# Performance work log

Measured on AMD Instinct MI355X. Metric: run time of the kernel, lower is better.

## Reference

```python
import jax, jax.numpy as jnp
import numpy as np

H = W = 192
C = 256
MAX_FEATURES = 2048
NUM_UP = 4  # num_upsampling scaling steps: pos -> pos*2 + 0.5 each step

# HandcraftedLocalizationModule filters (D2-Net)
DI  = [[0., -0.5, 0.], [0., 0., 0.], [0., 0.5, 0.]]
DJ  = [[0., 0., 0.], [-0.5, 0., 0.5], [0., 0., 0.]]
DII = [[0., 1., 0.], [0., -2., 0.], [0., 1., 0.]]
DJJ = [[0., 0., 0.], [1., -2., 1.], [0., 0., 0.]]
DIJ = [[0.25, 0., -0.25], [0., 0., 0.], [-0.25, 0., 0.25]]


def _conv3(x, k):
    # x: [H,W]; 3x3 cross-correlation, padding 1 (matches F.conv2d)
    k = jnp.asarray(k, x.dtype)
    return jax.lax.conv_general_dilated(x[None, None], k[None, None],
                                        window_strides=(1, 1),
                                        padding=[(1, 1), (1, 1)])[0, 0]


def _process_scale(feat, score):
    # feat: [C,H,W] dense descriptors, score: [H,W] attention/detection map
    Hm, Wm = score.shape
    # --- NMS: 3x3 maxpool, keep only local maxima (x[lmax != x] = 0) ---
    lmax = jax.lax.reduce_window(score, -jnp.inf, jax.lax.max,
                                 (3, 3), (1, 1), [(1, 1), (1, 1)])
    det = jnp.where(lmax == score, score, 0.0)
    valid = det != 0.0  # torch.nonzero equivalent (fixed-shape mask)
    # --- handcrafted localization (2x2 Newton step on the raw score map) ---
    di, dj = _conv3(score, DI), _conv3(score, DJ)
    dii, djj, dij = _conv3(score, DII), _conv3(score, DJJ), _conv3(score, DIJ)
    dd = dii * djj - dij * dij
    dd = jnp.where(dd == 0.0, 1e-20, dd)  # degenerate Hessian -> huge step, rejected by |.|<0.5
    step_i = -(djj * di - dij * dj) / dd
    step_j = -(-dij * di + dii * dj) / dd
    valid &= (jnp.abs(step_i) < 0.5) & (jnp.abs(step_j) < 0.5)
    ii, jj = jnp.meshgrid(jnp.arange(Hm, dtype=score.dtype),
                          jnp.arange(Wm, dtype=score.dtype), indexing='ij')
    ki = jnp.where(valid, ii + step_i, 0.0)
    kj = jnp.where(valid, jj + step_j, 0.0)
    # --- bilinear interpolation of dense features at sub-pixel keypoints ---
    i0 = jnp.floor(ki)
    j0 = jnp.floor(kj)
    valid &= (i0 >= 0) & (j0 >= 0) & (i0 + 1 <= Hm - 1) & (j0 + 1 <= Wm - 1)
    i0c = jnp.clip(i0, 0, Hm - 2).astype(jnp.int32)
    j0c = jnp.clip(j0, 0, Wm - 2).astype(jnp.int32)
    wi = ki - i0c
    wj = kj - j0c
    desc = (feat[:, i0c, j0c] * (1 - wi) * (1 - wj)
            + feat[:, i0c, j0c + 1] * (1 - wi) * wj
            + feat[:, i0c + 1, j0c] * wi * (1 - wj)
            + feat[:, i0c + 1, j0c + 1] * wi * wj)  # [C,H,W]
    norm = jnp.maximum(jnp.sqrt(jnp.sum(desc * desc, axis=0)), 1e-12)
    desc = desc / norm  # F.normalize(dim=0)
    # --- upscale positions: pos = pos*2 + 0.5 repeated NUM_UP times ---
    for _ in range(NUM_UP):
        ki = ki * 2 + 0.5
        kj = kj * 2 + 0.5
    scores = jnp.where(valid, det, -jnp.inf)  # invalid padded with -inf
    kp = jnp.stack([kj, ki], axis=-1).reshape(-1, 2)  # [:, [1,0]] swap -> (x, y)
    return kp, desc.reshape(desc.shape[0], -1).T, scores.reshape(-1), det


def setup_inputs() -> dict:
    key = jax.random.key(0)
    ks = jax.random.split(key, 6)
    return {
        "feat_early": jax.random.normal(ks[0], (1, C, H, W), jnp.float32),
        "feat_middle": jax.random.normal(ks[1], (1, C, H, W), jnp.float32),
        "feat_deep": jax.random.normal(ks[2], (1, C, H, W), jnp.float32),
        "score_early": jax.random.uniform(ks[3], (1, 1, H, W), jnp.float32),
        "score_middle": jax.random.uniform(ks[4], (1, 1, H, W), jnp.float32),
        "score_deep": jax.random.uniform(ks[5], (1, 1, H, W), jnp.float32),
    }


def reference(feat_early, feat_middle, feat_deep, score_early, score_middle, score_deep):
    feats = [feat_early[0], feat_middle[0], feat_deep[0]]
    smaps = [score_early[0, 0], score_middle[0, 0], score_deep[0, 0]]
    kps, descs, scs, dets = zip(*[_process_scale(f, s) for f, s in zip(feats, smaps)])
    kp = jnp.concatenate(kps)      # [3HW, 2]
    desc = jnp.concatenate(descs)  # [3HW, C]
    sc = jnp.concatenate(scs)      # [3HW]
    # torch.sort(descending) + thresh/max_features cap == top_k over padded scores
    top_s, idx = jax.lax.top_k(sc, MAX_FEATURES)
    sel = jnp.isfinite(top_s)
    keypoints = jnp.where(sel[:, None], kp[idx], 0.0)
    descriptors = jnp.where(sel[:, None], desc[idx], 0.0)
    scores = jnp.where(sel, top_s, 0.0)
    return keypoints, descriptors, scores, dets[0], dets[1], dets[2]
```

## Files before the change

### kernel.cpp

```cpp
#include <hip/hip_runtime.h>

#pragma clang fp contract(off)

#define H_ 192
#define W_ 192
#define HW_ (192 * 192)
#define NSC 3
#define NCAND (NSC * HW_)
#define CCH 256
#define KMAX 2048
#define NBIN 4096

#define KP_OFF 0
#define DESC_OFF (KMAX * 2)
#define SC_OFF (DESC_OFF + KMAX * CCH)
#define DET_OFF (SC_OFF + KMAX)

typedef unsigned long long u64;
typedef unsigned int u32;

#define CNT_OFF 884736
#define GH_OFF 884800
#define CUR_OFF 901184
#define SURV_OFF 917568
#define ZERO_BYTES 32832

__device__ __forceinline__ u32 key_bin(u32 sb) {
    if (sb >= 0xBF800000u) return NBIN - 1;
    if (sb >= 0xBF000000u) return 2048u + ((sb >> 12) & 0x7FFu);
    return (sb >> 20) & 0x7FFu;
}

__device__ __forceinline__ void newton_pixel(const float* __restrict__ sm, int i, int j,
                                             float& det, float& ki, float& kj, bool& valid) {
    float v[3][3];
#pragma unroll
    for (int a = 0; a < 3; ++a) {
#pragma unroll
        for (int b = 0; b < 3; ++b) {
            int ii = i + a - 1, jj = j + b - 1;
            bool in = (ii >= 0) && (ii < H_) && (jj >= 0) && (jj < W_);
            v[a][b] = in ? sm[ii * W_ + jj] : 0.0f;
        }
    }
    float c = v[1][1];
    float mx = v[0][0];
    mx = fmaxf(mx, v[0][1]); mx = fmaxf(mx, v[0][2]);
    mx = fmaxf(mx, v[1][0]); mx = fmaxf(mx, c);
    mx = fmaxf(mx, v[1][2]); mx = fmaxf(mx, v[2][0]);
    mx = fmaxf(mx, v[2][1]); mx = fmaxf(mx, v[2][2]);
    det = (mx == c) ? c : 0.0f;
    float di  = -0.5f * v[0][1] + 0.5f * v[2][1];
    float dj  = -0.5f * v[1][0] + 0.5f * v[1][2];
    float dii = v[0][1] - 2.0f * c + v[2][1];
    float djj = v[1][0] - 2.0f * c + v[1][2];
    float dij = 0.25f * v[0][0] - 0.25f * v[0][2] - 0.25f * v[2][0] + 0.25f * v[2][2];
    float dd = dii * djj - dij * dij;
    if (dd == 0.0f) dd = 1e-20f;
    float step_i = -(djj * di - dij * dj) / dd;
    float step_j = -(-dij * di + dii * dj) / dd;
    valid = (det != 0.0f) && (fabsf(step_i) < 0.5f) && (fabsf(step_j) < 0.5f);
    ki = valid ? ((float)i + step_i) : 0.0f;
    kj = valid ? ((float)j + step_j) : 0.0f;
    float i0 = floorf(ki), j0 = floorf(kj);
    valid = valid && (i0 >= 0.0f) && (j0 >= 0.0f) &&
            (i0 + 1.0f <= (float)(H_ - 1)) && (j0 + 1.0f <= (float)(W_ - 1));
}

__device__ __forceinline__ void decode_gid(u32 gid, int& s, int& i, int& j) {
    s = (int)(gid / HW_);
    int rem = (int)gid - s * HW_;
    i = rem / W_;
    j = rem - i * W_;
}

__device__ __forceinline__ void lds_suffix_scan(const u32* __restrict__ ghist,
                                                u32* ls, u32* lT) {
    int t = threadIdx.x;
    u32 chunk[16];
    u32 acc = 0;
#pragma unroll
    for (int k = 15; k >= 0; --k) {
        acc += ghist[t * 16 + k];
        chunk[k] = acc;
    }
    lT[t] = acc;
    __syncthreads();
    for (int off = 1; off < 256; off <<= 1) {
        u32 v = lT[t] + ((t + off < 256) ? lT[t + off] : 0u);
        __syncthreads();
        lT[t] = v;
        __syncthreads();
    }
    u32 add = (t < 255) ? lT[t + 1] : 0u;
#pragma unroll
    for (int k = 0; k < 16; ++k) ls[t * 16 + k] = chunk[k] + add;
    if (t == 0) ls[NBIN] = 0;
    __syncthreads();
}

__global__ __launch_bounds__(256) void cand_kernel(
    const float* __restrict__ s0, const float* __restrict__ s1, const float* __restrict__ s2,
    float* __restrict__ out, u64* __restrict__ fin, u32* __restrict__ cnts,
    u32* __restrict__ ghist) {
    __shared__ u32 lcnt, base;
    int tid = threadIdx.x;
    if (tid == 0) lcnt = 0;
    __syncthreads();
    int t = blockIdx.x * 256 + tid;
    bool valid = false;
    u64 key = 0;
    {
        int s, i, j;
        decode_gid((u32)t, s, i, j);
        const float* sm = (s == 0) ? s0 : (s == 1) ? s1 : s2;
        float det, ki, kj;
        newton_pixel(sm, i, j, det, ki, kj, valid);
        out[DET_OFF + t] = det;
        if (valid) {
            u32 sb = __float_as_uint(det) | 0x80000000u;
            key = ((u64)sb << 32) | (u64)(0xFFFFFFFFu - (u32)t);
            atomicAdd(&ghist[key_bin(sb)], 1u);
        }
    }
    u32 lpos = 0;
    if (valid) lpos = atomicAdd(&lcnt, 1u);
    __syncthreads();
    if (tid == 0 && lcnt > 0) base = atomicAdd(&cnts[0], lcnt);
    __syncthreads();
    if (valid) fin[base + lpos] = key;
}

__global__ __launch_bounds__(256) void scatter_kernel(
    const u64* __restrict__ fin, const u32* __restrict__ ghist, u32* __restrict__ cursor,
    const u32* __restrict__ cnts, u64* __restrict__ surv) {
    __shared__ u32 ls[NBIN + 1];
    __shared__ u32 lT[256];
    lds_suffix_scan(ghist, ls, lT);
    u32 n = cnts[0];
    for (u32 idx = blockIdx.x * 256 + threadIdx.x; idx < n; idx += 64 * 256) {
        u64 key = fin[idx];
        u32 b = key_bin((u32)(key >> 32));
        u32 seglo = ls[b + 1];
        if (seglo < KMAX) {
            u32 off = atomicAdd(&cursor[b], 1u);
            surv[seglo + off] = key;
        }
    }
}

__global__ __launch_bounds__(256) void output_kernel(
    const u64* __restrict__ surv, const u32* __restrict__ ghist,
    const float* __restrict__ s0, const float* __restrict__ s1, const float* __restrict__ s2,
    const float* __restrict__ f0, const float* __restrict__ f1, const float* __restrict__ f2,
    float* __restrict__ out) {
    __shared__ u32 ls[NBIN + 1];
    __shared__ u32 lT[256];
    lds_suffix_scan(ghist, ls, lT);
    int tid = threadIdx.x;
    int lane = tid & 63;
    int r = blockIdx.x * 4 + (tid >> 6);
    u32 n = ls[0];
    u32 nwin = (n < KMAX) ? n : KMAX;
    if ((u32)r >= nwin) {
#pragma unroll
        for (int k = 0; k < 4; ++k) out[DESC_OFF + r * CCH + k * 64 + lane] = 0.0f;
        if (lane == 0) {
            out[SC_OFF + r] = 0.0f;
            out[KP_OFF + r * 2 + 0] = 0.0f;
            out[KP_OFF + r * 2 + 1] = 0.0f;
        }
        return;
    }
    u32 blo = 0, bhi = NBIN;
    while (bhi - blo > 1) {
        u32 mid = (blo + bhi) >> 1;
        if (ls[mid] > (u32)r) blo = mid; else bhi = mid;
    }
    u32 b = blo;
    u32 seglo = ls[b + 1], seghi = ls[b];
    u64 mykey = 0;
    bool mine = false;
    for (u32 p = seglo + (u32)lane; p < seghi; p += 64) {
        u64 key = surv[p];
        u32 rk = seglo;
        for (u32 q = seglo; q < seghi; ++q) rk += (surv[q] > key) ? 1u : 0u;
        if (rk == (u32)r) { mykey = key; mine = true; }
    }
    u64 bal = __ballot(mine);
    int src = __ffsll((unsigned long long)bal) - 1;
    u32 klo = (u32)__shfl((int)(u32)(mykey & 0xFFFFFFFFull), src, 64);
    u32 khi = (u32)__shfl((int)(u32)(mykey >> 32), src, 64);
    u64 key = ((u64)khi << 32) | (u64)klo;
    u32 gid = 0xFFFFFFFFu - (u32)(key & 0xFFFFFFFFull);
    int s, i, j;
    decode_gid(gid, s, i, j);
    const float* sm = (s == 0) ? s0 : (s == 1) ? s1 : s2;
    float det, ki, kj;
    bool valid;
    newton_pixel(sm, i, j, det, ki, kj, valid);
    const float* feat = (s == 0) ? f0 : (s == 1) ? f1 : f2;
    int i0 = (int)floorf(ki), j0 = (int)floorf(kj);
    float wi = ki - (float)i0;
    float wj = kj - (float)j0;
    const float* p = feat + (size_t)lane * HW_ + i0 * W_ + j0;
    float d[4];
    float sq = 0.0f;
#pragma unroll
    for (int k = 0; k < 4; ++k) {
        const float* q = p + (size_t)k * 64 * HW_;
        float f00 = q[0], f01 = q[1], f10 = q[W_], f11 = q[W_ + 1];
        d[k] = f00 * (1.0f - wi) * (1.0f - wj) + f01 * (1.0f - wi) * wj +
               f10 * wi * (1.0f - wj) + f11 * wi * wj;
        sq += d[k] * d[k];
    }
#pragma unroll
    for (int o = 1; o < 64; o <<= 1) sq += __shfl_xor(sq, o, 64);
    float norm = fmaxf(sqrtf(sq), 1e-12f);
#pragma unroll
    for (int k = 0; k < 4; ++k)
        out[DESC_OFF + r * CCH + k * 64 + lane] = d[k] / norm;
    if (lane == 0) {
        float x = kj, y = ki;
#pragma unroll
        for (int u = 0; u < 4; ++u) { x = x * 2.0f + 0.5f; y = y * 2.0f + 0.5f; }
        out[SC_OFF + r] = det;
        out[KP_OFF + r * 2 + 0] = x;
        out[KP_OFF + r * 2 + 1] = y;
    }
}

extern "C" void kernel_launch(void* const* d_in, const int* in_sizes, int n_in,
                              void* d_out, int out_size, void* d_ws, size_t ws_size,
                              hipStream_t stream) {
    const float* f0 = (const float*)d_in[0];
    const float* f1 = (const float*)d_in[1];
    const float* f2 = (const float*)d_in[2];
    const float* s0 = (const float*)d_in[3];
    const float* s1 = (const float*)d_in[4];
    const float* s2 = (const float*)d_in[5];
    float* out = (float*)d_out;

    char* ws = (char*)d_ws;
    u64* fin = (u64*)ws;
    u32* cnts = (u32*)(ws + CNT_OFF);
    u32* ghist = (u32*)(ws + GH_OFF);
    u32* cursor = (u32*)(ws + CUR_OFF);
    u64* surv = (u64*)(ws + SURV_OFF);

    hipMemsetAsync(ws + CNT_OFF, 0, ZERO_BYTES, stream);
    cand_kernel<<<NCAND / 256, 256, 0, stream>>>(s0, s1, s2, out, fin, cnts, ghist);
    scatter_kernel<<<64, 256, 0, stream>>>(fin, ghist, cursor, cnts, surv);
    output_kernel<<<KMAX / 4, 256, 0, stream>>>(surv, ghist, s0, s1, s2, f0, f1, f2, out);
}
```

Baseline: 156.8 us.

## Drop scatter kernel; gather each wave's bin segment from candidates into LDS

Removes the separate scatter kernel and its global cursor and survivor buffers. Each wave in the output kernel now scans the full candidate list, filters keys that fall in its target histogram bin, and stages them in shared memory for the rank search. A serial arg-max fallback handles bins larger than the shared buffer. This saves one launch and the global atomic scatter, but every wave rereads all candidates and the larger shared allocation may reduce occupancy.

Result: slower. 208.2 us (+32.8%).

```diff
diff --git a/kernel.cpp b/kernel.cpp
--- a/kernel.cpp
+++ b/kernel.cpp
@@ -10,6 +10,7 @@
 #define CCH 256
 #define KMAX 2048
 #define NBIN 4096
+#define SEGCAP 1024
 
 #define KP_OFF 0
 #define DESC_OFF (KMAX * 2)
@@ -21,9 +22,7 @@
 
 #define CNT_OFF 884736
 #define GH_OFF 884800
-#define CUR_OFF 901184
-#define SURV_OFF 917568
-#define ZERO_BYTES 32832
+#define ZERO_BYTES 16448
 
 __device__ __forceinline__ u32 key_bin(u32 sb) {
     if (sb >= 0xBF800000u) return NBIN - 1;
@@ -131,35 +130,20 @@
     if (valid) fin[base + lpos] = key;
 }
 
-__global__ __launch_bounds__(256) void scatter_kernel(
-    const u64* __restrict__ fin, const u32* __restrict__ ghist, u32* __restrict__ cursor,
-    const u32* __restrict__ cnts, u64* __restrict__ surv) {
-    __shared__ u32 ls[NBIN + 1];
-    __shared__ u32 lT[256];
-    lds_suffix_scan(ghist, ls, lT);
-    u32 n = cnts[0];
-    for (u32 idx = blockIdx.x * 256 + threadIdx.x; idx < n; idx += 64 * 256) {
-        u64 key = fin[idx];
-        u32 b = key_bin((u32)(key >> 32));
-        u32 seglo = ls[b + 1];
-        if (seglo < KMAX) {
-            u32 off = atomicAdd(&cursor[b], 1u);
-            surv[seglo + off] = key;
-        }
-    }
-}
-
 __global__ __launch_bounds__(256) void output_kernel(
-    const u64* __restrict__ surv, const u32* __restrict__ ghist,
+    const u64* __restrict__ fin, const u32* __restrict__ ghist,
     const float* __restrict__ s0, const float* __restrict__ s1, const float* __restrict__ s2,
     const float* __restrict__ f0, const float* __restrict__ f1, const float* __restrict__ f2,
     float* __restrict__ out) {
     __shared__ u32 ls[NBIN + 1];
     __shared__ u32 lT[256];
+    __shared__ u64 seg[4][SEGCAP];
+    __shared__ u32 segcnt[4];
     lds_suffix_scan(ghist, ls, lT);
     int tid = threadIdx.x;
     int lane = tid & 63;
-    int r = blockIdx.x * 4 + (tid >> 6);
+    int w = tid >> 6;
+    int r = blockIdx.x * 4 + w;
     u32 n = ls[0];
     u32 nwin = (n < KMAX) ? n : KMAX;
     if ((u32)r >= nwin) {
@@ -179,19 +163,53 @@
     }
     u32 b = blo;
     u32 seglo = ls[b + 1], seghi = ls[b];
-    u64 mykey = 0;
-    bool mine = false;
-    for (u32 p = seglo + (u32)lane; p < seghi; p += 64) {
-        u64 key = surv[p];
-        u32 rk = seglo;
-        for (u32 q = seglo; q < seghi; ++q) rk += (surv[q] > key) ? 1u : 0u;
-        if (rk == (u32)r) { mykey = key; mine = true; }
-    }
-    u64 bal = __ballot(mine);
-    int src = __ffsll((unsigned long long)bal) - 1;
-    u32 klo = (u32)__shfl((int)(u32)(mykey & 0xFFFFFFFFull), src, 64);
-    u32 khi = (u32)__shfl((int)(u32)(mykey >> 32), src, 64);
-    u64 key = ((u64)khi << 32) | (u64)klo;
+    u32 segsz = seghi - seglo;
+    if (lane == 0) segcnt[w] = 0;
+    __builtin_amdgcn_wave_barrier();
+    u64 key;
+    if (segsz <= SEGCAP) {
+        for (u32 p = (u32)lane; p < n; p += 64) {
+            u64 k = fin[p];
+            if (key_bin((u32)(k >> 32)) == b) {
+                u32 pos = atomicAdd(&segcnt[w], 1u);
+                seg[w][pos] = k;
+            }
+        }
+        __builtin_amdgcn_wave_barrier();
+        __asm__ volatile("s_waitcnt lgkmcnt(0)");
+        u64 mykey = 0;
+        bool mine = false;
+        for (u32 idx = (u32)lane; idx < segsz; idx += 64) {
+            u64 k = seg[w][idx];
+            u32 rk = seglo;
+            for (u32 q = 0; q < segsz; ++q) rk += (seg[w][q] > k) ? 1u : 0u;
+            if (rk == (u32)r) { mykey = k; mine = true; }
+        }
+        u64 bal = __ballot(mine);
+        int src = __ffsll((unsigned long long)bal) - 1;
+        u32 klo = (u32)__shfl((int)(u32)(mykey & 0xFFFFFFFFull), src, 64);
+        u32 khi = (u32)__shfl((int)(u32)(mykey >> 32), src, 64);
+        key = ((u64)khi << 32) | (u64)klo;
+    } else {
+        u32 t_rank = (u32)r - seglo;
+        u64 cur = 0xFFFFFFFFFFFFFFFFull;
+        for (u32 it = 0; it <= t_rank; ++it) {
+            u64 best = 0;
+            for (u32 p = (u32)lane; p < n; p += 64) {
+                u64 k = fin[p];
+                if (key_bin((u32)(k >> 32)) == b && k < cur && k > best) best = k;
+            }
+#pragma unroll
+            for (int o = 1; o < 64; o <<= 1) {
+                u32 blo2 = (u32)__shfl_xor((int)(u32)(best & 0xFFFFFFFFull), o, 64);
+                u32 bhi2 = (u32)__shfl_xor((int)(u32)(best >> 32), o, 64);
+                u64 other = ((u64)bhi2 << 32) | (u64)blo2;
+                if (other > best) best = other;
+            }
+            cur = best;
+        }
+        key = cur;
+    }
     u32 gid = 0xFFFFFFFFu - (u32)(key & 0xFFFFFFFFull);
     int s, i, j;
     decode_gid(gid, s, i, j);
@@ -245,11 +263,8 @@
     u64* fin = (u64*)ws;
     u32* cnts = (u32*)(ws + CNT_OFF);
     u32* ghist = (u32*)(ws + GH_OFF);
-    u32* cursor = (u32*)(ws + CUR_OFF);
-    u64* surv = (u64*)(ws + SURV_OFF);
 
     hipMemsetAsync(ws + CNT_OFF, 0, ZERO_BYTES, stream);
     cand_kernel<<<NCAND / 256, 256, 0, stream>>>(s0, s1, s2, out, fin, cnts, ghist);
-    scatter_kernel<<<64, 256, 0, stream>>>(fin, ghist, cursor, cnts, surv);
-    output_kernel<<<KMAX / 4, 256, 0, stream>>>(surv, ghist, s0, s1, s2, f0, f1, f2, out);
-}
+    output_kernel<<<KMAX / 4, 256, 0, stream>>>(fin, ghist, s0, s1, s2, f0, f1, f2, out);
+}
```
